# Kernel tuning notes

Measured on AMD Instinct MI355X. Metric: run time of the kernel, lower is better.

## Reference

```python
import jax, jax.numpy as jnp
import numpy as np
from jax import lax
from math import sqrt

STYLE_DIM = 512
K = 3


def _equal_linear(latent, w, b):
    # EqualLinear: runtime weight scaling by 1/sqrt(fan_in)
    scale = 1.0 / sqrt(latent.shape[1])
    return latent @ (w.T * scale) + b


def _pixel_norm(x, axis=1, eps=1e-8):
    return x * jax.lax.rsqrt(jnp.mean(x * x, axis=axis, keepdims=True) + eps)


def _modconv(x, latent, weight, bias, el_w, el_b):
    # weight: (nc2, nc1, 3, 3); x: (B, nc1, H, W); latent: (B, style_dim)
    b = x.shape[0]
    nc2, nc1, k, _ = weight.shape
    fan_in = nc1 * k * k
    w = weight * sqrt(2.0 / fan_in)                      # (nc2, nc1, 3, 3)
    # style: s = 1 + PixelNorm(EqualLinear(latent))      # (B, nc1)
    s = 1.0 + _pixel_norm(_equal_linear(latent, el_w, el_b), axis=1)
    # demod: d_bo = rsqrt(sum_{c,k} (s_bc * w_ock)^2 + 1e-5)
    wsq = jnp.sum(w * w, axis=(2, 3))                    # (nc2, nc1)
    d = jax.lax.rsqrt(jnp.einsum('bc,oc->bo', s * s, wsq) + 1e-5)  # (B, nc2)
    # conv(x, s*w)*d  ==  conv(s*x, w)*d  (s is per input channel)
    xm = x * s[:, :, None, None]
    y = lax.conv_general_dilated(
        xm, w, window_strides=(1, 1), padding=[(1, 1), (1, 1)],
        dimension_numbers=('NCHW', 'OIHW', 'NCHW'))
    return y * d[:, :, None, None] + bias


def _style_block(x, latent, w0, b0, el0_w, el0_b, w1, b1, el1_w, el1_b):
    act_gain = sqrt(2.0)
    out = _modconv(x, latent, w0, b0, el0_w, el0_b)
    out = jax.nn.leaky_relu(out, 0.2) * act_gain
    out = _pixel_norm(out, axis=1)
    out = _modconv(out, latent, w1, b1, el1_w, el1_b)
    out = jax.nn.leaky_relu(out, 0.2) * act_gain
    out = _pixel_norm(out, axis=1)
    return out


def setup_inputs() -> dict:
    key = jax.random.key(0)
    ks = jax.random.split(key, 8)
    B, NC1, NC2, H, W = 8, 256, 256, 128, 128
    return {
        'x': jax.random.normal(ks[0], (B, NC1, H, W), jnp.float32),
        'latent': jax.random.normal(ks[1], (B, STYLE_DIM), jnp.float32),
        'w0': jax.random.normal(ks[2], (NC2, NC1, K, K), jnp.float32),
        'b0': jnp.zeros((1, NC2, 1, 1), jnp.float32),
        'el0_w': jax.random.normal(ks[3], (NC1, STYLE_DIM), jnp.float32),
        'el0_b': jnp.zeros((NC1,), jnp.float32),
        'w1': jax.random.normal(ks[4], (NC2, NC2, K, K), jnp.float32),
        'b1': jnp.zeros((1, NC2, 1, 1), jnp.float32),
        'el1_w': jax.random.normal(ks[5], (NC2, STYLE_DIM), jnp.float32),
        'el1_b': jnp.zeros((NC2,), jnp.float32),
    }


def reference(x, latent, w0, b0, el0_w, el0_b, w1, b1, el1_w, el1_b):
    return _style_block(x, latent, w0, b0, el0_w, el0_b, w1, b1, el1_w, el1_b)
```

## Files before the change

kernel.cpp:

```cpp
#include <hip/hip_runtime.h>
#include <hip/hip_bf16.h>

typedef __attribute__((ext_vector_type(8))) short short8;
typedef __attribute__((ext_vector_type(16))) float f32x16;

typedef const __attribute__((address_space(1))) unsigned int* gas1_t;
typedef __attribute__((address_space(3))) unsigned int* las3_t;

__device__ __forceinline__ unsigned short f2bf(float x) {
    unsigned int u = __float_as_uint(x);
    u = (u + 0x7fffu + ((u >> 16) & 1u)) >> 16;
    return (unsigned short)u;
}

__device__ __forceinline__ int4 pack8(const unsigned short* u) {
    int4 p;
    p.x = (int)((unsigned)u[0] | ((unsigned)u[1] << 16));
    p.y = (int)((unsigned)u[2] | ((unsigned)u[3] << 16));
    p.z = (int)((unsigned)u[4] | ((unsigned)u[5] << 16));
    p.w = (int)((unsigned)u[6] | ((unsigned)u[7] << 16));
    return p;
}

__device__ __forceinline__ void gld_lds16(const void* g, void* l) {
    __builtin_amdgcn_global_load_lds((gas1_t)g, (las3_t)l, 16, 0, 0);
}

__global__ void style_kernel(const float* __restrict__ latent,
                             const float* __restrict__ elw0, const float* __restrict__ elb0,
                             const float* __restrict__ elw1, const float* __restrict__ elb1,
                             float* __restrict__ s_arr) {
    const int cv = blockIdx.x >> 3;
    const int b  = blockIdx.x & 7;
    const int c  = threadIdx.x;
    const float* elw = cv ? elw1 : elw0;
    const float* elb = cv ? elb1 : elb0;

    __shared__ float lat[512];
    lat[c] = latent[b * 512 + c];
    lat[c + 256] = latent[b * 512 + c + 256];
    __syncthreads();

    float accv = 0.f;
    const float* wrow = elw + (size_t)c * 512;
#pragma unroll 8
    for (int k = 0; k < 512; ++k) accv += lat[k] * wrow[k];
    const float lin = accv * 0.04419417382415922f + elb[c];

    float sq = lin * lin;
#pragma unroll
    for (int off = 32; off >= 1; off >>= 1) sq += __shfl_xor(sq, off);
    __shared__ float wsum[4];
    if ((threadIdx.x & 63) == 0) wsum[threadIdx.x >> 6] = sq;
    __syncthreads();
    const float total = wsum[0] + wsum[1] + wsum[2] + wsum[3];
    const float s = 1.0f + lin * rsqrtf(total * (1.0f / 256.0f) + 1e-8f);
    s_arr[(cv * 8 + b) * 256 + c] = s;
}

__global__ void wsq_kernel(const float* __restrict__ w0, const float* __restrict__ w1,
                           float* __restrict__ wsq) {
    const int cv = blockIdx.x >> 8;
    const int o  = blockIdx.x & 255;
    const int c  = threadIdx.x;
    const float* w = cv ? w1 : w0;
    const size_t base = ((size_t)o * 256 + c) * 9;
    float ssum = 0.f;
#pragma unroll
    for (int t = 0; t < 9; ++t) { float v = w[base + t]; ssum += v * v; }
    wsq[((size_t)cv * 256 + o) * 256 + c] = ssum * (2.0f / 2304.0f);
}

__global__ void demod_kernel(const float* __restrict__ s_arr, const float* __restrict__ wsq,
                             float* __restrict__ d_arr) {
    const int cv = blockIdx.x >> 3;
    const int b  = blockIdx.x & 7;
    const int o  = threadIdx.x;
    __shared__ float ss[256];
    float sv = s_arr[(cv * 8 + b) * 256 + o];
    ss[o] = sv * sv;
    __syncthreads();
    const float* wrow = wsq + ((size_t)cv * 256 + o) * 256;
    float accv = 0.f;
#pragma unroll 8
    for (int c = 0; c < 256; ++c) accv += ss[c] * wrow[c];
    d_arr[(cv * 8 + b) * 256 + o] = rsqrtf(accv + 1e-5f);
}

__global__ void fold_kernel(const float* __restrict__ w0, const float* __restrict__ w1,
                            const float* __restrict__ s_arr, const float* __restrict__ d_arr,
                            unsigned short* __restrict__ wm0, unsigned short* __restrict__ wm1) {
    const int cv = blockIdx.y;
    const int e  = blockIdx.x * 256 + threadIdx.x;
    const float* w = cv ? w1 : w0;
    unsigned short* wm = cv ? wm1 : wm0;
    const int slab = e >> 13;
    const int idx  = e & 8191;
    const int b  = slab / 72;
    const int s2 = slab - b * 72;
    const int cc = s2 / 9;
    const int t  = s2 - cc * 9;
    const int o  = idx >> 5;
    const int c5 = idx & 31;
    const int c  = cc * 32 + c5;
    const float val = w[((size_t)o * 256 + c) * 9 + t] * 0.029462782549439483f
                    * s_arr[(cv * 8 + b) * 256 + c] * d_arr[(cv * 8 + b) * 256 + o];
    wm[((size_t)slab << 13) + (c5 >> 3) * 2048 + o * 8 + (c5 & 7)] = f2bf(val);
}

__global__ void convert_kernel(const float* __restrict__ x, unsigned short* __restrict__ xq) {
    const int blk = blockIdx.x;
    const int hh  = blk & 127;
    const int bg_ = blk >> 7;
    const int g   = bg_ & 31;
    const int b   = bg_ >> 5;
    __shared__ float sx[8][128];
    const int tid = threadIdx.x;
#pragma unroll
    for (int i = 0; i < 4; ++i) {
        const int idx = tid + i * 256;
        const int c8 = idx >> 7, p = idx & 127;
        sx[c8][p] = x[(((size_t)b * 256 + g * 8 + c8) * 128 + hh) * 128 + p];
    }
    __syncthreads();
    if (tid < 128) {
        const int p = tid;
        unsigned short u[8];
#pragma unroll
        for (int j = 0; j < 8; ++j) u[j] = f2bf(sx[j][p]);
        *(int4*)(xq + ((((size_t)b * 32 + g) * 128 + hh) * 128 + p) * 8) = pack8(u);
    }
}

template<bool FINAL_OUT>
__global__ __launch_bounds__(512, 2) void conv_kernel(
    const unsigned short* __restrict__ in_q, const unsigned short* __restrict__ wmod,
    const float* __restrict__ bias, const unsigned short* __restrict__ zpg,
    void* __restrict__ out_v) {

    __shared__ __align__(16) char lds[70720];

    const int tid  = threadIdx.x;
    const int b    = blockIdx.x & 7;
    const int rp   = blockIdx.x >> 3;
    const int h0   = rp * 2;
    const int lane = tid & 63;
    const int wr   = tid >> 6;
    const int wm   = wr & 3;
    const int wn   = wr >> 2;
    const int l31  = lane & 31;
    const int khg  = lane >> 5;

    float* sbias = (float*)(lds + 65600);
    if (tid < 256) sbias[tid] = bias[tid];
    if (tid < 4)   *(int4*)(lds + 65536 + tid * 16) = (int4){0, 0, 0, 0};

    const unsigned short* wmb = wmod + (size_t)b * 589824;
    const unsigned short* xqb = in_q + (size_t)b * 4194304;
    const char* aLane = (const char*)wmb + khg * 4096 + (wm * 64 + l31) * 16;

    auto issueB = [&](int cc, int buf) {
        const int chunk = tid >> 7, px = tid & 127;
#pragma unroll
        for (int r = 0; r < 4; ++r) {
            const int hin = h0 - 1 + r;
            const unsigned short* src = ((unsigned)hin < 128u)
                ? xqb + (((size_t)(cc * 4 + chunk) * 128 + hin) * 128 + px) * 8
                : zpg;
            gld_lds16(src, lds + buf * 32768 + r * 8192 + wr * 1024);
        }
    };

    short8 afA[2][2], afB[2][2];
    auto loadA = [&](int s, short8 (&af)[2][2]) {
        const char* p = aLane + (size_t)s * 16384;
        af[0][0] = *(const short8*)(p);
        af[1][0] = *(const short8*)(p + 512);
        af[0][1] = *(const short8*)(p + 8192);
        af[1][1] = *(const short8*)(p + 8704);
    };

    f32x16 acc[2][4];
#pragma unroll
    for (int mb = 0; mb < 2; ++mb)
#pragma unroll
        for (int nb = 0; nb < 4; ++nb)
#pragma unroll
            for (int r = 0; r < 16; ++r) acc[mb][nb][r] = 0.f;

    auto tap = [&](int s, short8 (&cur)[2][2], short8 (&nxt)[2][2]) {
        const int cc = s / 9;
        const int t  = s - cc * 9;
        if (t == 0) {
            if (s) {
                asm volatile("s_waitcnt vmcnt(0) lgkmcnt(0)" ::: "memory");
                __builtin_amdgcn_sched_barrier(0);
                __builtin_amdgcn_s_barrier();
            }
            if (cc < 7) issueB(cc + 1, (cc + 1) & 1);
        }
        if (s < 71) loadA(s + 1, nxt);

        const int dy = t / 3, dx = t - dy * 3;
        const int ob = (cc & 1) * 32768 + (wn + dy) * 8192 + khg * 2048 + (dx - 1) * 16;
        short8 bf[4][2];
#pragma unroll
        for (int nb = 0; nb < 4; ++nb)
#pragma unroll
            for (int kh = 0; kh < 2; ++kh) {
                int off = ob + kh * 4096 + (nb * 32 + l31) * 16;
                if (nb == 0) off = (l31 == 0 && dx == 0)  ? 65536 : off;
                if (nb == 3) off = (l31 == 31 && dx == 2) ? 65536 : off;
                bf[nb][kh] = *(const short8*)(lds + off);
            }
#pragma unroll
        for (int kh = 0; kh < 2; ++kh)
#pragma unroll
            for (int mb = 0; mb < 2; ++mb)
#pragma unroll
                for (int nb = 0; nb < 4; ++nb)
                    acc[mb][nb] = __builtin_amdgcn_mfma_f32_32x32x16_bf16(
                        cur[mb][kh], bf[nb][kh], acc[mb][nb], 0, 0, 0);
    };

    issueB(0, 0);
    loadA(0, afA);
    __syncthreads();

#pragma unroll 1
    for (int ss = 0; ss < 72; ss += 2) {
        tap(ss,     afA, afB);
        tap(ss + 1, afB, afA);
    }

    float psum[4] = {0.f, 0.f, 0.f, 0.f};
    const float actGain = 1.4142135623730951f;
#pragma unroll
    for (int mb = 0; mb < 2; ++mb)
#pragma unroll
        for (int rg = 0; rg < 16; ++rg) {
            const int row = (rg & 3) + 8 * (rg >> 2) + 4 * khg;
            const float bo = sbias[wm * 64 + mb * 32 + row];
#pragma unroll
            for (int nb = 0; nb < 4; ++nb) {
                float v = acc[mb][nb][rg] + bo;
                v = (v > 0.f ? v : 0.2f * v) * actGain;
                acc[mb][nb][rg] = v;
                psum[nb] += v * v;
            }
        }
#pragma unroll
    for (int nb = 0; nb < 4; ++nb) psum[nb] += __shfl_xor(psum[nb], 32);
    float* red = (float*)(lds + 66624);
    if (lane < 32) {
#pragma unroll
        for (int nb = 0; nb < 4; ++nb)
            red[(wn * 4 + wm) * 128 + nb * 32 + l31] = psum[nb];
    }
    __syncthreads();
    float rs[4];
#pragma unroll
    for (int nb = 0; nb < 4; ++nb) {
        const int p = nb * 32 + l31;
        const float ssum = red[(wn * 4 + 0) * 128 + p] + red[(wn * 4 + 1) * 128 + p]
                         + red[(wn * 4 + 2) * 128 + p] + red[(wn * 4 + 3) * 128 + p];
        rs[nb] = rsqrtf(ssum * (1.0f / 256.0f) + 1e-8f);
    }

    const int h = h0 + wn;
    if (FINAL_OUT) {
        float* outF = (float*)out_v;
#pragma unroll
        for (int mb = 0; mb < 2; ++mb)
#pragma unroll
            for (int rg = 0; rg < 16; ++rg) {
                const int row = (rg & 3) + 8 * (rg >> 2) + 4 * khg;
                const int o = wm * 64 + mb * 32 + row;
                const size_t rb = (((size_t)b * 256 + o) * 128 + h) * 128;
#pragma unroll
                for (int nb = 0; nb < 4; ++nb)
                    outF[rb + nb * 32 + l31] = acc[mb][nb][rg] * rs[nb];
            }
    } else {
        unsigned short* outB = (unsigned short*)out_v;
        char* wreg = lds + wr * 8192;
#pragma unroll
        for (int mb = 0; mb < 2; ++mb) {
#pragma unroll
            for (int rg = 0; rg < 16; rg += 2) {
                const int row = (rg & 3) + 8 * (rg >> 2) + 4 * khg;
#pragma unroll
                for (int nb = 0; nb < 4; ++nb) {
                    const int pxl = nb * 32 + l31;
                    const unsigned lo = f2bf(acc[mb][nb][rg]     * rs[nb]);
                    const unsigned hi = f2bf(acc[mb][nb][rg + 1] * rs[nb]);
                    *(unsigned int*)(wreg + pxl * 64 + (((row >> 3) ^ (pxl & 3)) << 4)
                                     + (row & 7) * 2) = lo | (hi << 16);
                }
            }
            asm volatile("s_waitcnt lgkmcnt(0)" ::: "memory");
#pragma unroll
            for (int oc = 0; oc < 4; ++oc)
#pragma unroll
                for (int ph = 0; ph < 2; ++ph) {
                    const int pxl = ph * 64 + lane;
                    const int4 v = *(const int4*)(wreg + pxl * 64 + ((oc ^ (pxl & 3)) << 4));
                    const int g = wm * 8 + mb * 4 + oc;
                    *(int4*)(outB + ((((size_t)b * 32 + g) * 128 + h) * 128 + pxl) * 8) = v;
                }
            asm volatile("s_waitcnt lgkmcnt(0)" ::: "memory");
        }
    }
}

extern "C" void kernel_launch(void* const* d_in, const int* in_sizes, int n_in,
                              void* d_out, int out_size, void* d_ws, size_t ws_size,
                              hipStream_t stream) {
    (void)in_sizes; (void)n_in; (void)out_size; (void)ws_size;
    const float* x      = (const float*)d_in[0];
    const float* latent = (const float*)d_in[1];
    const float* w0     = (const float*)d_in[2];
    const float* b0     = (const float*)d_in[3];
    const float* el0w   = (const float*)d_in[4];
    const float* el0b   = (const float*)d_in[5];
    const float* w1     = (const float*)d_in[6];
    const float* b1     = (const float*)d_in[7];
    const float* el1w   = (const float*)d_in[8];
    const float* el1b   = (const float*)d_in[9];

    char* ws = (char*)d_ws;
    float* s_arr = (float*)ws;
    float* d_arr = (float*)(ws + 16384);
    float* wsq   = (float*)(ws + 32768);
    unsigned short* zpg = (unsigned short*)(ws + 32768);
    unsigned short* wm0 = (unsigned short*)(ws + 557056);
    unsigned short* wm1 = (unsigned short*)(ws + 9994240);
    unsigned short* xq  = (unsigned short*)(ws + 19431424);
    unsigned short* tmp = (unsigned short*)(ws + 86540288);

    style_kernel<<<16, 256, 0, stream>>>(latent, el0w, el0b, el1w, el1b, s_arr);
    wsq_kernel<<<512, 256, 0, stream>>>(w0, w1, wsq);
    demod_kernel<<<16, 256, 0, stream>>>(s_arr, wsq, d_arr);
    hipMemsetAsync(zpg, 0, 256, stream);
    fold_kernel<<<dim3(18432, 2), 256, 0, stream>>>(w0, w1, s_arr, d_arr, wm0, wm1);
    convert_kernel<<<32768, 256, 0, stream>>>(x, xq);

    conv_kernel<false><<<512, 512, 0, stream>>>(xq, wm0, b0, zpg, tmp);
    conv_kernel<true><<<512, 512, 0, stream>>>(tmp, wm1, b1, zpg, d_out);
}
```

Before: 376.6 us.

## Shrink conv tile to one row half per block and raise occupancy

The conv kernel moves from 512-thread blocks covering two output rows × 128 pixels to 256-thread blocks covering one row × 64 pixels, launched as 2048 blocks instead of 512. LDS use and accumulator registers drop, so more blocks and waves can be resident per CU to hide latency. In exchange, modulated weights are reloaded four times as often per output pixel, and the input halo rows are re-fetched more. The MFMA section is also wrapped in s_setprio to favor issuing the math.

```diff
diff --git a/kernel.cpp b/kernel.cpp
--- a/kernel.cpp
+++ b/kernel.cpp
@@ -133,41 +133,47 @@
 }
 
 template<bool FINAL_OUT>
-__global__ __launch_bounds__(512, 2) void conv_kernel(
+__global__ __launch_bounds__(256, 3) void conv_kernel(
     const unsigned short* __restrict__ in_q, const unsigned short* __restrict__ wmod,
     const float* __restrict__ bias, const unsigned short* __restrict__ zpg,
     void* __restrict__ out_v) {
 
-    __shared__ __align__(16) char lds[70720];
+    __shared__ __align__(16) char lds[51264];
 
     const int tid  = threadIdx.x;
     const int b    = blockIdx.x & 7;
-    const int rp   = blockIdx.x >> 3;
-    const int h0   = rp * 2;
+    const int h    = (blockIdx.x >> 3) & 127;
+    const int half = blockIdx.x >> 10;
     const int lane = tid & 63;
     const int wr   = tid >> 6;
-    const int wm   = wr & 3;
-    const int wn   = wr >> 2;
+    const int wm   = wr;
     const int l31  = lane & 31;
     const int khg  = lane >> 5;
 
-    float* sbias = (float*)(lds + 65600);
-    if (tid < 256) sbias[tid] = bias[tid];
-    if (tid < 4)   *(int4*)(lds + 65536 + tid * 16) = (int4){0, 0, 0, 0};
+    float* sbias = (float*)(lds + 49216);
+    sbias[tid] = bias[tid];
+    if (tid < 4) *(int4*)(lds + 49152 + tid * 16) = (int4){0, 0, 0, 0};
 
     const unsigned short* wmb = wmod + (size_t)b * 589824;
     const unsigned short* xqb = in_q + (size_t)b * 4194304;
     const char* aLane = (const char*)wmb + khg * 4096 + (wm * 64 + l31) * 16;
 
     auto issueB = [&](int cc, int buf) {
-        const int chunk = tid >> 7, px = tid & 127;
-#pragma unroll
-        for (int r = 0; r < 4; ++r) {
-            const int hin = h0 - 1 + r;
-            const unsigned short* src = ((unsigned)hin < 128u)
-                ? xqb + (((size_t)(cc * 4 + chunk) * 128 + hin) * 128 + px) * 8
-                : zpg;
-            gld_lds16(src, lds + buf * 32768 + r * 8192 + wr * 1024);
+        const int px    = tid & 127;
+        const int kbase = tid >> 7;
+#pragma unroll
+        for (int r = 0; r < 3; ++r) {
+            const int hin = h + r - 1;
+            const bool ok = (unsigned)hin < 128u;
+#pragma unroll
+            for (int i = 0; i < 2; ++i) {
+                const int koct = i * 2 + kbase;
+                const unsigned short* src = ok
+                    ? xqb + (((size_t)(cc * 4 + koct) * 128 + hin) * 128 + px) * 8
+                    : zpg;
+                gld_lds16(src, lds + buf * 24576 + r * 8192 + koct * 2048
+                               + (wr & 1) * 1024);
+            }
         }
     };
 
@@ -180,11 +186,11 @@
         af[1][1] = *(const short8*)(p + 8704);
     };
 
-    f32x16 acc[2][4];
+    f32x16 acc[2][2];
 #pragma unroll
     for (int mb = 0; mb < 2; ++mb)
 #pragma unroll
-        for (int nb = 0; nb < 4; ++nb)
+        for (int nb = 0; nb < 2; ++nb)
 #pragma unroll
             for (int r = 0; r < 16; ++r) acc[mb][nb][r] = 0.f;
 
@@ -202,25 +208,28 @@
         if (s < 71) loadA(s + 1, nxt);
 
         const int dy = t / 3, dx = t - dy * 3;
-        const int ob = (cc & 1) * 32768 + (wn + dy) * 8192 + khg * 2048 + (dx - 1) * 16;
-        short8 bf[4][2];
-#pragma unroll
-        for (int nb = 0; nb < 4; ++nb)
+        const int ob = (cc & 1) * 24576 + dy * 8192 + khg * 2048
+                     + (half * 64 + dx - 1) * 16;
+        short8 bf[2][2];
+#pragma unroll
+        for (int nb = 0; nb < 2; ++nb)
 #pragma unroll
             for (int kh = 0; kh < 2; ++kh) {
                 int off = ob + kh * 4096 + (nb * 32 + l31) * 16;
-                if (nb == 0) off = (l31 == 0 && dx == 0)  ? 65536 : off;
-                if (nb == 3) off = (l31 == 31 && dx == 2) ? 65536 : off;
+                if (nb == 0 && dx == 0) off = (l31 == 0  && half == 0) ? 49152 : off;
+                if (nb == 1 && dx == 2) off = (l31 == 31 && half == 1) ? 49152 : off;
                 bf[nb][kh] = *(const short8*)(lds + off);
             }
+        __builtin_amdgcn_s_setprio(1);
 #pragma unroll
         for (int kh = 0; kh < 2; ++kh)
 #pragma unroll
             for (int mb = 0; mb < 2; ++mb)
 #pragma unroll
-                for (int nb = 0; nb < 4; ++nb)
+                for (int nb = 0; nb < 2; ++nb)
                     acc[mb][nb] = __builtin_amdgcn_mfma_f32_32x32x16_bf16(
                         cur[mb][kh], bf[nb][kh], acc[mb][nb], 0, 0, 0);
+        __builtin_amdgcn_s_setprio(0);
     };
 
     issueB(0, 0);
@@ -233,7 +242,7 @@
         tap(ss + 1, afB, afA);
     }
 
-    float psum[4] = {0.f, 0.f, 0.f, 0.f};
+    float psum[2] = {0.f, 0.f};
     const float actGain = 1.4142135623730951f;
 #pragma unroll
     for (int mb = 0; mb < 2; ++mb)
@@ -242,32 +251,29 @@
             const int row = (rg & 3) + 8 * (rg >> 2) + 4 * khg;
             const float bo = sbias[wm * 64 + mb * 32 + row];
 #pragma unroll
-            for (int nb = 0; nb < 4; ++nb) {
+            for (int nb = 0; nb < 2; ++nb) {
                 float v = acc[mb][nb][rg] + bo;
                 v = (v > 0.f ? v : 0.2f * v) * actGain;
                 acc[mb][nb][rg] = v;
                 psum[nb] += v * v;
             }
         }
-#pragma unroll
-    for (int nb = 0; nb < 4; ++nb) psum[nb] += __shfl_xor(psum[nb], 32);
-    float* red = (float*)(lds + 66624);
+    psum[0] += __shfl_xor(psum[0], 32);
+    psum[1] += __shfl_xor(psum[1], 32);
+    float* red = (float*)(lds + 50240);
     if (lane < 32) {
-#pragma unroll
-        for (int nb = 0; nb < 4; ++nb)
-            red[(wn * 4 + wm) * 128 + nb * 32 + l31] = psum[nb];
-    }
-    __syncthreads();
-    float rs[4];
-#pragma unroll
-    for (int nb = 0; nb < 4; ++nb) {
+        red[wr * 64 + l31]      = psum[0];
+        red[wr * 64 + 32 + l31] = psum[1];
+    }
+    __syncthreads();
+    float rs[2];
+#pragma unroll
+    for (int nb = 0; nb < 2; ++nb) {
         const int p = nb * 32 + l31;
-        const float ssum = red[(wn * 4 + 0) * 128 + p] + red[(wn * 4 + 1) * 128 + p]
-                         + red[(wn * 4 + 2) * 128 + p] + red[(wn * 4 + 3) * 128 + p];
+        const float ssum = red[p] + red[64 + p] + red[128 + p] + red[192 + p];
         rs[nb] = rsqrtf(ssum * (1.0f / 256.0f) + 1e-8f);
     }
 
-    const int h = h0 + wn;
     if (FINAL_OUT) {
         float* outF = (float*)out_v;
 #pragma unroll
@@ -276,21 +282,21 @@
             for (int rg = 0; rg < 16; ++rg) {
                 const int row = (rg & 3) + 8 * (rg >> 2) + 4 * khg;
                 const int o = wm * 64 + mb * 32 + row;
-                const size_t rb = (((size_t)b * 256 + o) * 128 + h) * 128;
-#pragma unroll
-                for (int nb = 0; nb < 4; ++nb)
+                const size_t rb = (((size_t)b * 256 + o) * 128 + h) * 128 + half * 64;
+#pragma unroll
+                for (int nb = 0; nb < 2; ++nb)
                     outF[rb + nb * 32 + l31] = acc[mb][nb][rg] * rs[nb];
             }
     } else {
         unsigned short* outB = (unsigned short*)out_v;
-        char* wreg = lds + wr * 8192;
+        char* wreg = lds + wr * 4096;
 #pragma unroll
         for (int mb = 0; mb < 2; ++mb) {
 #pragma unroll
             for (int rg = 0; rg < 16; rg += 2) {
                 const int row = (rg & 3) + 8 * (rg >> 2) + 4 * khg;
 #pragma unroll
-                for (int nb = 0; nb < 4; ++nb) {
+                for (int nb = 0; nb < 2; ++nb) {
                     const int pxl = nb * 32 + l31;
                     const unsigned lo = f2bf(acc[mb][nb][rg]     * rs[nb]);
                     const unsigned hi = f2bf(acc[mb][nb][rg + 1] * rs[nb]);
@@ -300,14 +306,13 @@
             }
             asm volatile("s_waitcnt lgkmcnt(0)" ::: "memory");
 #pragma unroll
-            for (int oc = 0; oc < 4; ++oc)
-#pragma unroll
-                for (int ph = 0; ph < 2; ++ph) {
-                    const int pxl = ph * 64 + lane;
-                    const int4 v = *(const int4*)(wreg + pxl * 64 + ((oc ^ (pxl & 3)) << 4));
-                    const int g = wm * 8 + mb * 4 + oc;
-                    *(int4*)(outB + ((((size_t)b * 32 + g) * 128 + h) * 128 + pxl) * 8) = v;
-                }
+            for (int oc = 0; oc < 4; ++oc) {
+                const int pxl = lane;
+                const int4 v = *(const int4*)(wreg + pxl * 64 + ((oc ^ (pxl & 3)) << 4));
+                const int g = wm * 8 + mb * 4 + oc;
+                *(int4*)(outB + ((((size_t)b * 32 + g) * 128 + h) * 128
+                                 + half * 64 + pxl) * 8) = v;
+            }
             asm volatile("s_waitcnt lgkmcnt(0)" ::: "memory");
         }
     }
@@ -345,6 +350,6 @@
     fold_kernel<<<dim3(18432, 2), 256, 0, stream>>>(w0, w1, s_arr, d_arr, wm0, wm1);
     convert_kernel<<<32768, 256, 0, stream>>>(x, xq);
 
-    conv_kernel<false><<<512, 512, 0, stream>>>(xq, wm0, b0, zpg, tmp);
-    conv_kernel<true><<<512, 512, 0, stream>>>(tmp, wm1, b1, zpg, d_out);
-}
+    conv_kernel<false><<<2048, 256, 0, stream>>>(xq, wm0, b0, zpg, tmp);
+    conv_kernel<true><<<2048, 256, 0, stream>>>(tmp, wm1, b1, zpg, d_out);
+}
```

Measured after the change: 429.5 us. 1.14x slower.
